# Performance work log

Measured on AMD Instinct MI355X. Metric: run time of the kernel, lower is better.

The kernel has to match this reference:

```python
import jax, jax.numpy as jnp
import numpy as np

B, T, N, L, D, H = 8, 6, 24, 1024, 512, 8
DH = D // H
EPS = 1e-5


def setup_inputs() -> dict:
    key = jax.random.key(0)
    ks = jax.random.split(key, 8)
    q = jax.random.normal(ks[0], (B, T, N, D), jnp.float32)
    k = jax.random.normal(ks[1], (B, T, L, D), jnp.float32)
    v = jax.random.normal(ks[2], (B, T, L, D), jnp.float32)
    attn_mask = jax.random.randint(ks[3], (T * N, T * L), 0, 10) == 0
    s = D ** -0.5
    Wq = jax.random.normal(ks[4], (D, D), jnp.float32) * s
    Wk = jax.random.normal(ks[5], (D, D), jnp.float32) * s
    Wv = jax.random.normal(ks[6], (D, D), jnp.float32) * s
    Wo = jax.random.normal(ks[7], (D, D), jnp.float32) * s
    return {"q": q, "k": k, "v": v, "attn_mask": attn_mask,
            "Wq": Wq, "Wk": Wk, "Wv": Wv, "Wo": Wo}


def reference(q, k, v, attn_mask, Wq, Wk, Wv, Wo):
    # Projections (torch Linear: y = x @ W.T), split into heads
    qp = (q.reshape(B, T * N, D) @ Wq.T).reshape(B, T * N, H, DH).transpose(0, 2, 1, 3)
    kp = (k.reshape(B, T * L, D) @ Wk.T).reshape(B, T * L, H, DH).transpose(0, 2, 1, 3)
    vp = (v.reshape(B, T * L, D) @ Wv.T).reshape(B, T * L, H, DH).transpose(0, 2, 1, 3)
    qp = qp * (DH ** -0.5)
    # scores: [B, H, T*N, T*L]
    scores = jnp.einsum('bhnd,bhmd->bhnm', qp, kp)
    scores = jnp.where(attn_mask[None, None], -jnp.inf, scores)
    # cross-head softmax: normalize over the combined (H*N) axis per (b, t, tl)
    a = scores.reshape(B, H, T, N, T * L).transpose(0, 2, 4, 1, 3)  # B,T,TL,H,N
    a = a.reshape(B, T, T * L, H * N)
    a = jax.nn.softmax(a, axis=-1)
    a = a.reshape(B, T, T * L, H, N).transpose(0, 3, 1, 4, 2).reshape(B, H, T * N, T * L)
    a = jnp.where(attn_mask[None, None], 0.0, a)
    attn_vis = a
    # renormalize along key axis
    a = a / (a.sum(axis=-1, keepdims=True) + EPS)
    out = jnp.einsum('bhnm,bhmd->bhnd', a, vp)  # B,H,T*N,DH
    out = out.transpose(0, 2, 1, 3).reshape(B, T * N, D)
    out = (out @ Wo.T).reshape(B, T, N, D)
    return out, attn_vis
```

## Files before the change

kernel.cpp:

```cpp
#include <hip/hip_runtime.h>
#include <hip/hip_bf16.h>
#include <math.h>

#define CB 8
#define CT 6
#define CN 24
#define CL 1024
#define CD 512
#define CH 8
#define CDH 64
#define CTN 144
#define CTL 6144
#define CMS 16
#define CEPS 1e-5f

typedef __bf16 bf16x8 __attribute__((ext_vector_type(8)));
typedef float  f32x4  __attribute__((ext_vector_type(4)));

#define MFMA16(a,b,c) __builtin_amdgcn_mfma_f32_16x16x32_bf16(a,b,c,0,0,0)

union BF8 { unsigned short s[8]; bf16x8 v; };

static __device__ __forceinline__ unsigned short f2bf(float x){
    union { float f; unsigned u; } c; c.f = x;
    return (unsigned short)((c.u + 0x7FFFu + ((c.u >> 16) & 1u)) >> 16);
}

static __device__ __forceinline__ float bf2f(unsigned short u){
    union { unsigned u; float f; } c; c.u = ((unsigned)u) << 16;
    return c.f;
}

static __device__ __forceinline__ bf16x8 pack8(f32x4 a, f32x4 b){
    BF8 r;
    r.s[0]=f2bf(a[0]); r.s[1]=f2bf(a[1]); r.s[2]=f2bf(a[2]); r.s[3]=f2bf(a[3]);
    r.s[4]=f2bf(b[0]); r.s[5]=f2bf(b[1]); r.s[6]=f2bf(b[2]); r.s[7]=f2bf(b[3]);
    return r.v;
}

static __device__ __forceinline__ bf16x8 ldbf8(const unsigned short* __restrict__ p){
    return *(const bf16x8*)p;
}

#define GL16(gp, lp) __builtin_amdgcn_global_load_lds((const unsigned int*)(gp), (unsigned int*)(lp), 16, 0, 0)

__global__ void cvt_w_kernel(const float* __restrict__ w0, const float* __restrict__ w1,
                             const float* __restrict__ w2, const float* __restrict__ w3,
                             unsigned short* __restrict__ o0, unsigned short* __restrict__ o1,
                             unsigned short* __restrict__ o2, unsigned short* __restrict__ o3){
    int i = blockIdx.x*blockDim.x + threadIdx.x;
    const int n = CD*CD;
    if      (i < n)   o0[i]       = f2bf(w0[i]);
    else if (i < 2*n) o1[i-n]     = f2bf(w1[i-n]);
    else if (i < 3*n) o2[i-2*n]   = f2bf(w2[i-2*n]);
    else if (i < 4*n) o3[i-3*n]   = f2bf(w3[i-3*n]);
}

__global__ void maskb_kernel(const int* __restrict__ mask, unsigned int* __restrict__ maskb){
    int i = blockIdx.x*blockDim.x + threadIdx.x;
    if (i >= CT*CTL) return;
    int t = i / CTL, m = i - t*CTL;
    unsigned w = 0;
    for (int n = 0; n < 24; ++n)
        if (mask[(size_t)(t*24 + n)*CTL + m] != 0) w |= (1u << n);
    maskb[i] = w;
}

template<int MODE, int AFMT>
__global__ __launch_bounds__(512, 4) void gemm_m97(
    const void* __restrict__ Ap, const unsigned short* __restrict__ W,
    void* __restrict__ outv, int posPer, int rowoff, float scale)
{
    __shared__ union {
        struct { unsigned short As[128*64]; unsigned short Bs[128*64]; } s;
        float epi[32][129];
    } sm;

    int nwg = gridDim.x*gridDim.y;
    int id  = blockIdx.y*gridDim.x + blockIdx.x;
    int q8 = nwg >> 3, r8 = nwg & 7;
    int xcd = id & 7, rk = id >> 3;
    int swz = (xcd < r8 ? xcd*(q8+1) : r8*(q8+1) + (xcd-r8)*q8) + rk;
    int ctile = swz & 3;
    int bt    = swz >> 2;

    int tid = threadIdx.x;
    int lane = tid & 63, wave = tid >> 6;
    int wr = wave >> 2, wc = wave & 3;
    int qq = lane & 15, g = lane >> 4;

    int sr = tid >> 3;
    int sc = (((tid & 7) ^ ((sr >> 1) & 7)) * 8);
    const unsigned short* gah = (const unsigned short*)Ap + (size_t)(bt*128 + sr)*CD + sc;
    const unsigned short* gb  = W + (size_t)(ctile*128 + sr)*CD + sc;
    unsigned short* lA = sm.s.As + wave*512;
    unsigned short* lB = sm.s.Bs + wave*512;

    int arow = tid >> 2;
    const float* gaf = (const float*)Ap + (size_t)(bt*128 + arow)*CD + (tid & 3)*16;
    int akey = (arow >> 1) & 7;
    int asl0 = (tid & 3)*2;
    unsigned short* aw0 = sm.s.As + arow*64 + ((asl0     ^ akey)*8);
    unsigned short* aw1 = sm.s.As + arow*64 + (((asl0|1) ^ akey)*8);

    f32x4 acc[4][2] = {};
    int s1 = (qq >> 1) & 7;

    for (int k0 = 0; k0 < CD; k0 += 64) {
        if (AFMT == 0) {
            f32x4 w0 = *(const f32x4*)(gaf + k0);
            f32x4 w1 = *(const f32x4*)(gaf + k0 + 4);
            f32x4 w2 = *(const f32x4*)(gaf + k0 + 8);
            f32x4 w3 = *(const f32x4*)(gaf + k0 + 12);
            *(bf16x8*)aw0 = pack8(w0, w1);
            *(bf16x8*)aw1 = pack8(w2, w3);
        } else {
            GL16(gah + k0,          lA);
            GL16(gah + 64*CD + k0,  lA + 4096);
        }
        GL16(gb + k0,          lB);
        GL16(gb + 64*CD + k0,  lB + 4096);
        __syncthreads();
        #pragma unroll
        for (int x = 0; x < 2; ++x) {
            int slot = ((x*4 + g) ^ s1) * 8;
            bf16x8 af[4], bf[2];
            #pragma unroll
            for (int mf = 0; mf < 4; ++mf)
                af[mf] = *(const bf16x8*)&sm.s.As[(wr*64 + mf*16 + qq)*64 + slot];
            #pragma unroll
            for (int nf = 0; nf < 2; ++nf)
                bf[nf] = *(const bf16x8*)&sm.s.Bs[(wc*32 + nf*16 + qq)*64 + slot];
            #pragma unroll
            for (int mf = 0; mf < 4; ++mf)
                #pragma unroll
                for (int nf = 0; nf < 2; ++nf)
                    acc[mf][nf] = MFMA16(af[mf], bf[nf], acc[mf][nf]);
        }
        __syncthreads();
    }

    unsigned short* outu = (unsigned short*)outv;
    float* outf = (float*)outv;
    for (int p = 0; p < 4; ++p) {
        if (wr == (p >> 1)) {
            #pragma unroll
            for (int mh = 0; mh < 2; ++mh) {
                int mf = (p&1)*2 + mh;
                #pragma unroll
                for (int nf = 0; nf < 2; ++nf)
                    #pragma unroll
                    for (int r = 0; r < 4; ++r)
                        sm.epi[mh*16 + 4*g + r][wc*32 + nf*16 + qq] = acc[mf][nf][r]*scale;
            }
        }
        __syncthreads();
        if (MODE == 1) {
            #pragma unroll
            for (int i = 0; i < 8; ++i) {
                int c2 = i*16 + wave*2 + (lane>>5);
                int gr = rowoff + bt*128 + p*32 + (lane & 31);
                int bb = gr / posPer, pos = gr - bb*posPer;
                int hh = ctile*2 + (c2>>6), dh = c2 & 63;
                outu[((size_t)(bb*CH + hh)*64 + dh)*posPer + pos] = f2bf(sm.epi[lane&31][c2]);
            }
        } else {
            #pragma unroll
            for (int i = 0; i < 8; ++i) {
                int task = i*8 + wave;
                int lr = task >> 1, ch = task & 1;
                float val = sm.epi[lr][ch*64 + lane];
                int gr = rowoff + bt*128 + p*32 + lr;
                if (MODE == 2) {
                    outf[(size_t)gr*CD + ctile*128 + ch*64 + lane] = val;
                } else {
                    int bb = gr / posPer, pos = gr - bb*posPer;
                    int hh = ctile*2 + ch;
                    outu[((size_t)(bb*CH + hh)*posPer + pos)*64 + lane] = f2bf(val);
                }
            }
        }
        __syncthreads();
    }
}

__global__ __launch_bounds__(256) void scores_a_kernel(
    const unsigned short* __restrict__ qp, const unsigned short* __restrict__ kp,
    const unsigned int* __restrict__ maskb,
    float* __restrict__ pmax, float* __restrict__ psum)
{
    __shared__ float S[CTN][65];
    int mt = blockIdx.x;
    int h = blockIdx.y, b = blockIdx.z;
    int lane = threadIdx.x & 63, wave = threadIdx.x >> 6;
    const unsigned short* qbase = qp + (size_t)(b*CH + h)*CTN*64;
    const unsigned short* kbase = kp + (size_t)(b*CH + h)*CTL*64;
    int koff = 8*(lane>>4);
    f32x4 acc[3][4] = {};
    for (int k0 = 0; k0 < 64; k0 += 32) {
        bf16x8 bfr[4];
        #pragma unroll
        for (int cf = 0; cf < 4; ++cf)
            bfr[cf] = ldbf8(kbase + (size_t)(mt*64 + cf*16 + (lane&15))*64 + k0 + koff);
        #pragma unroll
        for (int i = 0; i < 3; ++i) {
            int rt = wave + 4*i;
            if (rt < 9) {
                bf16x8 a = ldbf8(qbase + (size_t)(rt*16 + (lane&15))*64 + k0 + koff);
                #pragma unroll
                for (int cf = 0; cf < 4; ++cf)
                    acc[i][cf] = MFMA16(a, bfr[cf], acc[i][cf]);
            }
        }
    }
    #pragma unroll
    for (int i = 0; i < 3; ++i) {
        int rt = wave + 4*i;
        if (rt < 9) {
            #pragma unroll
            for (int cf = 0; cf < 4; ++cf)
                #pragma unroll
                for (int r = 0; r < 4; ++r)
                    S[rt*16 + 4*(lane>>4) + r][cf*16 + (lane&15)] = acc[i][cf][r];
        }
    }
    __syncthreads();
    int mg0 = mt*64;
    for (int task = threadIdx.x; task < CT*64; task += 256) {
        int t = task >> 6, ml = task & 63;
        int mg = mg0 + ml;
        unsigned w = maskb[(size_t)t*CTL + mg];
        float mx = -INFINITY;
        float sv[24];
        #pragma unroll
        for (int i = 0; i < 24; ++i) {
            float s = ((w >> i) & 1u) ? -INFINITY : S[t*24 + i][ml];
            sv[i] = s;
            mx = fmaxf(mx, s);
        }
        float sum = 0.f;
        if (mx > -INFINITY) {
            #pragma unroll
            for (int i = 0; i < 24; ++i)
                if (sv[i] > -INFINITY) sum += __expf(sv[i] - mx);
        }
        size_t idx = ((size_t)(b*CH + h)*CT + t)*CTL + mg;
        pmax[idx] = mx; psum[idx] = sum;
    }
}

__global__ void combine_kernel(const float* __restrict__ pmax, const float* __restrict__ psum,
                               const unsigned int* __restrict__ maskb,
                               float2* __restrict__ stat2){
    size_t i = (size_t)blockIdx.x*blockDim.x + threadIdx.x;
    if (i >= (size_t)CB*CT*CTL) return;
    int m = (int)(i % CTL);
    size_t bt = i / CTL;
    int t = (int)(bt % CT), b = (int)(bt / CT);
    float pm[CH], ps[CH];
    float mx = -INFINITY;
    #pragma unroll
    for (int h = 0; h < CH; ++h) {
        size_t idx = ((size_t)(b*CH + h)*CT + t)*CTL + m;
        pm[h] = pmax[idx]; ps[h] = psum[idx];
        mx = fmaxf(mx, pm[h]);
    }
    float s = 0.f;
    if (mx > -INFINITY) {
        #pragma unroll
        for (int h = 0; h < CH; ++h)
            if (pm[h] > -INFINITY) s += ps[h]*__expf(pm[h] - mx);
    }
    float lse = (mx > -INFINITY && s > 0.f) ? mx + __logf(s) : 0.f;
    float2 o; o.x = lse; o.y = __uint_as_float(maskb[(size_t)t*CTL + m]);
    stat2[i] = o;
}

__global__ __launch_bounds__(64, 3) void fused_bpv(
    const unsigned short* __restrict__ qp, const unsigned short* __restrict__ kp,
    const unsigned short* __restrict__ vpT,
    const float2* __restrict__ stat2,
    float* __restrict__ avis, unsigned short* __restrict__ pvpart,
    float* __restrict__ rowpart)
{
    __shared__ unsigned short abf[16][68];
    __shared__ float av32[16][65];

    int ms = blockIdx.x;
    int ry = blockIdx.y;
    int bh = blockIdx.z;
    int b = bh >> 3;
    int lane = threadIdx.x;
    int qq = lane & 15, g = lane >> 4;
    int koff = 8*g;
    int nrt = (ry < 4) ? 2 : 1;
    int rt0 = ry*2;

    const unsigned short* qbase = qp + (size_t)bh*CTN*64;
    const unsigned short* kbase = kp + (size_t)bh*CTL*64;
    const unsigned short* vb    = vpT + (size_t)bh*64*CTL;

    int rbit[2];
    const float2* stp[2];
    float* avbase[2];
    bf16x8 qf[2][2];
    #pragma unroll
    for (int i = 0; i < 2; ++i) {
        int rt = rt0 + ((i < 2) ? i : 0);
        if (i >= nrt) rt = rt0;
        int qrow = rt*16 + qq;
        int t = qrow / 24;
        rbit[i] = qrow - t*24;
        stp[i] = stat2 + (size_t)(b*CT + t)*CTL;
        avbase[i] = avis + ((size_t)bh*CTN + rt*16)*CTL;
        #pragma unroll
        for (int x = 0; x < 2; ++x)
            qf[i][x] = ldbf8(qbase + (size_t)qrow*64 + x*32 + koff);
    }

    f32x4 pv[2][4] = {};
    float rs[2] = {0.f, 0.f};

    for (int mt = 0; mt < 6; ++mt) {
        int mg0 = ms*384 + mt*64;
        bf16x8 vf[2][4];
        #pragma unroll
        for (int x = 0; x < 2; ++x)
            #pragma unroll
            for (int cf = 0; cf < 4; ++cf)
                vf[x][cf] = ldbf8(vb + (size_t)(cf*16 + qq)*CTL + mg0 + x*32 + koff);
        f32x4 sacc[2][4] = {};
        #pragma unroll
        for (int x = 0; x < 2; ++x) {
            bf16x8 kf[4];
            #pragma unroll
            for (int cf = 0; cf < 4; ++cf)
                kf[cf] = ldbf8(kbase + (size_t)(mg0 + cf*16 + qq)*64 + x*32 + koff);
            #pragma unroll
            for (int cf = 0; cf < 4; ++cf)
                sacc[0][cf] = MFMA16(kf[cf], qf[0][x], sacc[0][cf]);
            if (nrt == 2) {
                #pragma unroll
                for (int cf = 0; cf < 4; ++cf)
                    sacc[1][cf] = MFMA16(kf[cf], qf[1][x], sacc[1][cf]);
            }
        }
        #pragma unroll
        for (int i = 0; i < 2; ++i) {
            if (i < nrt) {
                #pragma unroll
                for (int cf = 0; cf < 4; ++cf) {
                    const f32x4* sp = (const f32x4*)(stp[i] + mg0 + cf*16 + 4*g);
                    f32x4 s0 = sp[0], s1 = sp[1];
                    f32x4 av;
                    av[0] = ((__float_as_uint(s0[1]) >> rbit[i]) & 1u) ? 0.f : __expf(sacc[i][cf][0] - s0[0]);
                    av[1] = ((__float_as_uint(s0[3]) >> rbit[i]) & 1u) ? 0.f : __expf(sacc[i][cf][1] - s0[2]);
                    av[2] = ((__float_as_uint(s1[1]) >> rbit[i]) & 1u) ? 0.f : __expf(sacc[i][cf][2] - s1[0]);
                    av[3] = ((__float_as_uint(s1[3]) >> rbit[i]) & 1u) ? 0.f : __expf(sacc[i][cf][3] - s1[2]);
                    *(f32x4*)&av32[qq][cf*16 + 4*g] = av;
                    unsigned short u4[4] = { f2bf(av[0]), f2bf(av[1]), f2bf(av[2]), f2bf(av[3]) };
                    *(unsigned long long*)&abf[qq][cf*16 + 4*g] = *(unsigned long long*)u4;
                    rs[i] += av[0] + av[1] + av[2] + av[3];
                }
                #pragma unroll
                for (int p = 0; p < 4; ++p) {
                    int row = 4*p + (lane >> 4);
                    int col = 4*(lane & 15);
                    f32x4 v4 = *(const f32x4*)&av32[row][col];
                    __builtin_nontemporal_store(v4, (f32x4*)(avbase[i] + (size_t)row*CTL + mg0 + col));
                }
                #pragma unroll
                for (int x = 0; x < 2; ++x) {
                    bf16x8 af = *(const bf16x8*)&abf[qq][x*32 + koff];
                    #pragma unroll
                    for (int cf = 0; cf < 4; ++cf)
                        pv[i][cf] = MFMA16(af, vf[x][cf], pv[i][cf]);
                }
            }
        }
    }

    #pragma unroll
    for (int i = 0; i < 2; ++i) {
        if (i < nrt) {
            int rt = rt0 + i;
            float s = rs[i];
            s += __shfl_xor(s, 16);
            s += __shfl_xor(s, 32);
            if (g == 0)
                rowpart[(size_t)ms*(CB*CH*CTN) + (size_t)bh*CTN + rt*16 + qq] = s;
            unsigned short* pb = pvpart + ((size_t)(ms*64 + bh)*CTN + rt*16)*64;
            #pragma unroll
            for (int cf = 0; cf < 4; ++cf) {
                unsigned short u4[4] = { f2bf(pv[i][cf][0]), f2bf(pv[i][cf][1]),
                                         f2bf(pv[i][cf][2]), f2bf(pv[i][cf][3]) };
                *(unsigned long long*)&pb[cf*256 + lane*4] = *(unsigned long long*)u4;
            }
        }
    }
}

__global__ void pv_reduce_kernel(const unsigned short* __restrict__ pvpart,
                                 const float* __restrict__ rowpart,
                                 unsigned short* __restrict__ oh){
    int idx = blockIdx.x*blockDim.x + threadIdx.x;
    if (idx >= CB*CH*CTN*64) return;
    int col = idx & 63;
    int rowbh = idx >> 6;
    int row = rowbh % CTN, bh = rowbh / CTN;
    float rsum = 0.f;
    #pragma unroll
    for (int ms = 0; ms < CMS; ++ms)
        rsum += rowpart[(size_t)ms*(CB*CH*CTN) + rowbh];
    int rt = row >> 4, lr = row & 15, g = lr >> 2, r = lr & 3;
    int cf = col >> 4, qq = col & 15;
    size_t off = ((size_t)bh*CTN + rt*16)*64 + cf*256 + (g*16 + qq)*4 + r;
    float s = 0.f;
    #pragma unroll
    for (int ms = 0; ms < CMS; ++ms)
        s += bf2f(pvpart[(size_t)ms*((size_t)CB*CH*CTN*64) + off]);
    float inv = 1.f / (rsum + CEPS);
    int b = bh >> 3, h = bh & 7;
    oh[((size_t)b*CTN + row)*CD + h*64 + col] = f2bf(s*inv);
}

extern "C" void kernel_launch(void* const* d_in, const int* in_sizes, int n_in,
                              void* d_out, int out_size, void* d_ws, size_t ws_size,
                              hipStream_t stream)
{
    const float* q    = (const float*)d_in[0];
    const float* k    = (const float*)d_in[1];
    const float* v    = (const float*)d_in[2];
    const int*   mask = (const int*)  d_in[3];
    const float* Wq   = (const float*)d_in[4];
    const float* Wk   = (const float*)d_in[5];
    const float* Wv   = (const float*)d_in[6];
    const float* Wo   = (const float*)d_in[7];

    float* out0 = (float*)d_out;
    float* avis = out0 + (size_t)CB*CTN*CD;

    char* p = (char*)d_ws;
    auto alloc = [&](size_t bytes) -> char* {
        char* r = p; p += (bytes + 255) & ~(size_t)255; return r;
    };
    unsigned short* Wq_bf = (unsigned short*)alloc((size_t)CD*CD*2);
    unsigned short* Wk_bf = (unsigned short*)alloc((size_t)CD*CD*2);
    unsigned short* Wv_bf = (unsigned short*)alloc((size_t)CD*CD*2);
    unsigned short* Wo_bf = (unsigned short*)alloc((size_t)CD*CD*2);
    unsigned short* qp    = (unsigned short*)alloc((size_t)CB*CH*CTN*64*2);
    unsigned short* kp    = (unsigned short*)alloc((size_t)CB*CH*CTL*64*2);
    unsigned short* vpT   = (unsigned short*)alloc((size_t)CB*CH*64*CTL*2);
    char* S = alloc((size_t)CB*CH*CT*CTL*4*2);
    float* pmax   = (float*)S;
    float* psum   = (float*)(S + (size_t)CB*CH*CT*CTL*4);
    unsigned short* pvpart = (unsigned short*)S;
    float2* stat2 = (float2*)alloc((size_t)CB*CT*CTL*8);
    unsigned int* maskb = (unsigned int*)alloc((size_t)CT*CTL*4);
    float* rowpart = (float*)alloc((size_t)CMS*CB*CH*CTN*4);
    unsigned short* oh = (unsigned short*)alloc((size_t)CB*CTN*CD*2);

    cvt_w_kernel<<<(4*CD*CD + 255)/256, 256, 0, stream>>>(Wq, Wk, Wv, Wo,
                                                          Wq_bf, Wk_bf, Wv_bf, Wo_bf);
    maskb_kernel<<<(CT*CTL + 255)/256, 256, 0, stream>>>(mask, maskb);
    gemm_m97<0,0><<<dim3(4, CB*CTN/128), 512, 0, stream>>>(q, Wq_bf, qp, CTN, 0, 0.125f);
    gemm_m97<0,0><<<dim3(4, CB*CTL/128), 512, 0, stream>>>(k, Wk_bf, kp, CTL, 0, 1.0f);
    gemm_m97<1,0><<<dim3(4, CB*CTL/128), 512, 0, stream>>>(v, Wv_bf, vpT, CTL, 0, 1.0f);
    scores_a_kernel<<<dim3(CTL/64, CH, CB), 256, 0, stream>>>(qp, kp, maskb, pmax, psum);
    combine_kernel<<<((CB*CT*CTL) + 255)/256, 256, 0, stream>>>(pmax, psum, maskb, stat2);
    fused_bpv<<<dim3(CMS, 5, CB*CH), 64, 0, stream>>>(qp, kp, vpT, stat2,
                                                      avis, pvpart, rowpart);
    pv_reduce_kernel<<<((CB*CH*CTN*64) + 255)/256, 256, 0, stream>>>(pvpart, rowpart, oh);
    gemm_m97<2,1><<<dim3(4, CB*CTN/128), 512, 0, stream>>>(oh, Wo_bf, out0, CD, 0, 1.0f);
}
```

Baseline: 436.7 us.

## Rebalance scores and fused attention kernels into uniform 3-row-tile blocks

The scores kernel is split so each block handles two time steps (48 query rows) with three waves instead of all 144 rows with four waves. This triples the grid and shrinks shared memory per block. The fused softmax/PV kernel now gives each block three full row tiles (3 y-blocks instead of 5 uneven ones), which removes the nrt branching and reuses each loaded K/V fragment across more rows. The cost is higher register pressure, so the occupancy hint drops from 3 to 2 blocks per CU, and the scores kernel reloads K tiles three times more often.

```diff
diff --git a/kernel.cpp b/kernel.cpp
--- a/kernel.cpp
+++ b/kernel.cpp
@@ -184,57 +184,48 @@
     }
 }
 
-__global__ __launch_bounds__(256) void scores_a_kernel(
+__global__ __launch_bounds__(192) void scores_a_kernel(
     const unsigned short* __restrict__ qp, const unsigned short* __restrict__ kp,
     const unsigned int* __restrict__ maskb,
     float* __restrict__ pmax, float* __restrict__ psum)
 {
-    __shared__ float S[CTN][65];
+    __shared__ float S[48][65];
     int mt = blockIdx.x;
-    int h = blockIdx.y, b = blockIdx.z;
+    int tg = blockIdx.y;
+    int bh = blockIdx.z;
     int lane = threadIdx.x & 63, wave = threadIdx.x >> 6;
-    const unsigned short* qbase = qp + (size_t)(b*CH + h)*CTN*64;
-    const unsigned short* kbase = kp + (size_t)(b*CH + h)*CTL*64;
-    int koff = 8*(lane>>4);
-    f32x4 acc[3][4] = {};
+    int qq = lane & 15, g = lane >> 4;
+    int koff = 8*g;
+    const unsigned short* qbase = qp + (size_t)bh*CTN*64;
+    const unsigned short* kbase = kp + (size_t)bh*CTL*64;
+
+    f32x4 acc[4] = {};
     for (int k0 = 0; k0 < 64; k0 += 32) {
-        bf16x8 bfr[4];
-        #pragma unroll
-        for (int cf = 0; cf < 4; ++cf)
-            bfr[cf] = ldbf8(kbase + (size_t)(mt*64 + cf*16 + (lane&15))*64 + k0 + koff);
-        #pragma unroll
-        for (int i = 0; i < 3; ++i) {
-            int rt = wave + 4*i;
-            if (rt < 9) {
-                bf16x8 a = ldbf8(qbase + (size_t)(rt*16 + (lane&15))*64 + k0 + koff);
-                #pragma unroll
-                for (int cf = 0; cf < 4; ++cf)
-                    acc[i][cf] = MFMA16(a, bfr[cf], acc[i][cf]);
-            }
-        }
-    }
-    #pragma unroll
-    for (int i = 0; i < 3; ++i) {
-        int rt = wave + 4*i;
-        if (rt < 9) {
-            #pragma unroll
-            for (int cf = 0; cf < 4; ++cf)
-                #pragma unroll
-                for (int r = 0; r < 4; ++r)
-                    S[rt*16 + 4*(lane>>4) + r][cf*16 + (lane&15)] = acc[i][cf][r];
-        }
-    }
+        bf16x8 a = ldbf8(qbase + (size_t)(tg*48 + wave*16 + qq)*64 + k0 + koff);
+        #pragma unroll
+        for (int cf = 0; cf < 4; ++cf) {
+            bf16x8 bfr = ldbf8(kbase + (size_t)(mt*64 + cf*16 + qq)*64 + k0 + koff);
+            acc[cf] = MFMA16(a, bfr, acc[cf]);
+        }
+    }
+    #pragma unroll
+    for (int cf = 0; cf < 4; ++cf)
+        #pragma unroll
+        for (int r = 0; r < 4; ++r)
+            S[wave*16 + 4*g + r][cf*16 + qq] = acc[cf][r];
     __syncthreads();
-    int mg0 = mt*64;
-    for (int task = threadIdx.x; task < CT*64; task += 256) {
-        int t = task >> 6, ml = task & 63;
-        int mg = mg0 + ml;
+
+    int task = threadIdx.x;
+    if (task < 128) {
+        int lt = task >> 6, ml = task & 63;
+        int t = tg*2 + lt;
+        int mg = mt*64 + ml;
         unsigned w = maskb[(size_t)t*CTL + mg];
         float mx = -INFINITY;
         float sv[24];
         #pragma unroll
         for (int i = 0; i < 24; ++i) {
-            float s = ((w >> i) & 1u) ? -INFINITY : S[t*24 + i][ml];
+            float s = ((w >> i) & 1u) ? -INFINITY : S[lt*24 + i][ml];
             sv[i] = s;
             mx = fmaxf(mx, s);
         }
@@ -244,7 +235,7 @@
             for (int i = 0; i < 24; ++i)
                 if (sv[i] > -INFINITY) sum += __expf(sv[i] - mx);
         }
-        size_t idx = ((size_t)(b*CH + h)*CT + t)*CTL + mg;
+        size_t idx = ((size_t)bh*CT + t)*CTL + mg;
         pmax[idx] = mx; psum[idx] = sum;
     }
 }
@@ -276,7 +267,7 @@
     stat2[i] = o;
 }
 
-__global__ __launch_bounds__(64, 3) void fused_bpv(
+__global__ __launch_bounds__(64, 2) void fused_bpv(
     const unsigned short* __restrict__ qp, const unsigned short* __restrict__ kp,
     const unsigned short* __restrict__ vpT,
     const float2* __restrict__ stat2,
@@ -293,21 +284,19 @@
     int lane = threadIdx.x;
     int qq = lane & 15, g = lane >> 4;
     int koff = 8*g;
-    int nrt = (ry < 4) ? 2 : 1;
-    int rt0 = ry*2;
+    int rt0 = ry*3;
 
     const unsigned short* qbase = qp + (size_t)bh*CTN*64;
     const unsigned short* kbase = kp + (size_t)bh*CTL*64;
     const unsigned short* vb    = vpT + (size_t)bh*64*CTL;
 
-    int rbit[2];
-    const float2* stp[2];
-    float* avbase[2];
-    bf16x8 qf[2][2];
-    #pragma unroll
-    for (int i = 0; i < 2; ++i) {
-        int rt = rt0 + ((i < 2) ? i : 0);
-        if (i >= nrt) rt = rt0;
+    int rbit[3];
+    const float2* stp[3];
+    float* avbase[3];
+    bf16x8 qf[3][2];
+    #pragma unroll
+    for (int i = 0; i < 3; ++i) {
+        int rt = rt0 + i;
         int qrow = rt*16 + qq;
         int t = qrow / 24;
         rbit[i] = qrow - t*24;
@@ -318,8 +307,8 @@
             qf[i][x] = ldbf8(qbase + (size_t)qrow*64 + x*32 + koff);
     }
 
-    f32x4 pv[2][4] = {};
-    float rs[2] = {0.f, 0.f};
+    f32x4 pv[3][4] = {};
+    float rs[3] = {0.f, 0.f, 0.f};
 
     for (int mt = 0; mt < 6; ++mt) {
         int mg0 = ms*384 + mt*64;
@@ -329,7 +318,7 @@
             #pragma unroll
             for (int cf = 0; cf < 4; ++cf)
                 vf[x][cf] = ldbf8(vb + (size_t)(cf*16 + qq)*CTL + mg0 + x*32 + koff);
-        f32x4 sacc[2][4] = {};
+        f32x4 sacc[3][4] = {};
         #pragma unroll
         for (int x = 0; x < 2; ++x) {
             bf16x8 kf[4];
@@ -337,65 +326,58 @@
             for (int cf = 0; cf < 4; ++cf)
                 kf[cf] = ldbf8(kbase + (size_t)(mg0 + cf*16 + qq)*64 + x*32 + koff);
             #pragma unroll
-            for (int cf = 0; cf < 4; ++cf)
-                sacc[0][cf] = MFMA16(kf[cf], qf[0][x], sacc[0][cf]);
-            if (nrt == 2) {
+            for (int i = 0; i < 3; ++i)
                 #pragma unroll
                 for (int cf = 0; cf < 4; ++cf)
-                    sacc[1][cf] = MFMA16(kf[cf], qf[1][x], sacc[1][cf]);
-            }
-        }
-        #pragma unroll
-        for (int i = 0; i < 2; ++i) {
-            if (i < nrt) {
+                    sacc[i][cf] = MFMA16(kf[cf], qf[i][x], sacc[i][cf]);
+        }
+        #pragma unroll
+        for (int i = 0; i < 3; ++i) {
+            #pragma unroll
+            for (int cf = 0; cf < 4; ++cf) {
+                const f32x4* sp = (const f32x4*)(stp[i] + mg0 + cf*16 + 4*g);
+                f32x4 s0 = sp[0], s1 = sp[1];
+                f32x4 av;
+                av[0] = ((__float_as_uint(s0[1]) >> rbit[i]) & 1u) ? 0.f : __expf(sacc[i][cf][0] - s0[0]);
+                av[1] = ((__float_as_uint(s0[3]) >> rbit[i]) & 1u) ? 0.f : __expf(sacc[i][cf][1] - s0[2]);
+                av[2] = ((__float_as_uint(s1[1]) >> rbit[i]) & 1u) ? 0.f : __expf(sacc[i][cf][2] - s1[0]);
+                av[3] = ((__float_as_uint(s1[3]) >> rbit[i]) & 1u) ? 0.f : __expf(sacc[i][cf][3] - s1[2]);
+                *(f32x4*)&av32[qq][cf*16 + 4*g] = av;
+                unsigned short u4[4] = { f2bf(av[0]), f2bf(av[1]), f2bf(av[2]), f2bf(av[3]) };
+                *(unsigned long long*)&abf[qq][cf*16 + 4*g] = *(unsigned long long*)u4;
+                rs[i] += av[0] + av[1] + av[2] + av[3];
+            }
+            #pragma unroll
+            for (int p = 0; p < 4; ++p) {
+                int row = 4*p + (lane >> 4);
+                int col = 4*(lane & 15);
+                f32x4 v4 = *(const f32x4*)&av32[row][col];
+                __builtin_nontemporal_store(v4, (f32x4*)(avbase[i] + (size_t)row*CTL + mg0 + col));
+            }
+            #pragma unroll
+            for (int x = 0; x < 2; ++x) {
+                bf16x8 af = *(const bf16x8*)&abf[qq][x*32 + koff];
                 #pragma unroll
-                for (int cf = 0; cf < 4; ++cf) {
-                    const f32x4* sp = (const f32x4*)(stp[i] + mg0 + cf*16 + 4*g);
-                    f32x4 s0 = sp[0], s1 = sp[1];
-                    f32x4 av;
-                    av[0] = ((__float_as_uint(s0[1]) >> rbit[i]) & 1u) ? 0.f : __expf(sacc[i][cf][0] - s0[0]);
-                    av[1] = ((__float_as_uint(s0[3]) >> rbit[i]) & 1u) ? 0.f : __expf(sacc[i][cf][1] - s0[2]);
-                    av[2] = ((__float_as_uint(s1[1]) >> rbit[i]) & 1u) ? 0.f : __expf(sacc[i][cf][2] - s1[0]);
-                    av[3] = ((__float_as_uint(s1[3]) >> rbit[i]) & 1u) ? 0.f : __expf(sacc[i][cf][3] - s1[2]);
-                    *(f32x4*)&av32[qq][cf*16 + 4*g] = av;
-                    unsigned short u4[4] = { f2bf(av[0]), f2bf(av[1]), f2bf(av[2]), f2bf(av[3]) };
-                    *(unsigned long long*)&abf[qq][cf*16 + 4*g] = *(unsigned long long*)u4;
-                    rs[i] += av[0] + av[1] + av[2] + av[3];
-                }
-                #pragma unroll
-                for (int p = 0; p < 4; ++p) {
-                    int row = 4*p + (lane >> 4);
-                    int col = 4*(lane & 15);
-                    f32x4 v4 = *(const f32x4*)&av32[row][col];
-                    __builtin_nontemporal_store(v4, (f32x4*)(avbase[i] + (size_t)row*CTL + mg0 + col));
-                }
-                #pragma unroll
-                for (int x = 0; x < 2; ++x) {
-                    bf16x8 af = *(const bf16x8*)&abf[qq][x*32 + koff];
-                    #pragma unroll
-                    for (int cf = 0; cf < 4; ++cf)
-                        pv[i][cf] = MFMA16(af, vf[x][cf], pv[i][cf]);
-                }
-            }
-        }
-    }
-
-    #pragma unroll
-    for (int i = 0; i < 2; ++i) {
-        if (i < nrt) {
-            int rt = rt0 + i;
-            float s = rs[i];
-            s += __shfl_xor(s, 16);
-            s += __shfl_xor(s, 32);
-            if (g == 0)
-                rowpart[(size_t)ms*(CB*CH*CTN) + (size_t)bh*CTN + rt*16 + qq] = s;
-            unsigned short* pb = pvpart + ((size_t)(ms*64 + bh)*CTN + rt*16)*64;
-            #pragma unroll
-            for (int cf = 0; cf < 4; ++cf) {
-                unsigned short u4[4] = { f2bf(pv[i][cf][0]), f2bf(pv[i][cf][1]),
-                                         f2bf(pv[i][cf][2]), f2bf(pv[i][cf][3]) };
-                *(unsigned long long*)&pb[cf*256 + lane*4] = *(unsigned long long*)u4;
-            }
+                for (int cf = 0; cf < 4; ++cf)
+                    pv[i][cf] = MFMA16(af, vf[x][cf], pv[i][cf]);
+            }
+        }
+    }
+
+    #pragma unroll
+    for (int i = 0; i < 3; ++i) {
+        int rt = rt0 + i;
+        float s = rs[i];
+        s += __shfl_xor(s, 16);
+        s += __shfl_xor(s, 32);
+        if (g == 0)
+            rowpart[(size_t)ms*(CB*CH*CTN) + (size_t)bh*CTN + rt*16 + qq] = s;
+        unsigned short* pb = pvpart + ((size_t)(ms*64 + bh)*CTN + rt*16)*64;
+        #pragma unroll
+        for (int cf = 0; cf < 4; ++cf) {
+            unsigned short u4[4] = { f2bf(pv[i][cf][0]), f2bf(pv[i][cf][1]),
+                                     f2bf(pv[i][cf][2]), f2bf(pv[i][cf][3]) };
+            *(unsigned long long*)&pb[cf*256 + lane*4] = *(unsigned long long*)u4;
         }
     }
 }
@@ -466,9 +448,9 @@
     gemm_m97<0,0><<<dim3(4, CB*CTN/128), 512, 0, stream>>>(q, Wq_bf, qp, CTN, 0, 0.125f);
     gemm_m97<0,0><<<dim3(4, CB*CTL/128), 512, 0, stream>>>(k, Wk_bf, kp, CTL, 0, 1.0f);
     gemm_m97<1,0><<<dim3(4, CB*CTL/128), 512, 0, stream>>>(v, Wv_bf, vpT, CTL, 0, 1.0f);
-    scores_a_kernel<<<dim3(CTL/64, CH, CB), 256, 0, stream>>>(qp, kp, maskb, pmax, psum);
+    scores_a_kernel<<<dim3(CTL/64, 3, CB*CH), 192, 0, stream>>>(qp, kp, maskb, pmax, psum);
     combine_kernel<<<((CB*CT*CTL) + 255)/256, 256, 0, stream>>>(pmax, psum, maskb, stat2);
-    fused_bpv<<<dim3(CMS, 5, CB*CH), 64, 0, stream>>>(qp, kp, vpT, stat2,
+    fused_bpv<<<dim3(CMS, 3, CB*CH), 64, 0, stream>>>(qp, kp, vpT, stat2,
                                                       avis, pvpart, rowpart);
     pv_reduce_kernel<<<((CB*CH*CTN*64) + 255)/256, 256, 0, stream>>>(pvpart, rowpart, oh);
     gemm_m97<2,1><<<dim3(4, CB*CTN/128), 512, 0, stream>>>(oh, Wo_bf, out0, CD, 0, 1.0f);
```

New measurement: 455.7 us. 1.04x slower.
